# Kernel optimization log

Hardware: AMD Instinct MI355X
Metric: run time of the kernel (lower is better)

Reference implementation:

```python
import jax, jax.numpy as jnp
import numpy as np
from jax import lax

FILTER_SIZE = 11
N_ITER = 5


def gaussian_kernel1d(inv_theta, spacing, size):
    # distances = spacing * [-(size//2) .. size//2]; zero out center tap
    d = spacing * jnp.arange(-(size // 2), size // 2 + 1, dtype=jnp.float32)
    k = jnp.exp(-(d * inv_theta) ** 2 / 2)
    return k.at[size // 2].set(0.0)


def conv_along_axis(x, kernel, axis):
    # x: (C, *spatial); 1D conv along `axis`, 'same' padding (kernel symmetric -> corr == conv)
    x = jnp.moveaxis(x, axis, -1)
    shp = x.shape
    x2 = x.reshape(-1, 1, shp[-1])  # (M, 1, L)
    K = kernel.shape[0]
    out = lax.conv_general_dilated(
        x2, kernel[None, None, :].astype(x2.dtype), (1,), [(K // 2, K // 2)],
        dimension_numbers=('NCH', 'OIH', 'NCH'))
    return jnp.moveaxis(out.reshape(shp), -1, axis)


def _gaussian_filter_single(xi, inv_theta, spacing):
    # xi: (C, H, W); separable gaussian with per-sample spacing
    for i in range(2):
        k = gaussian_kernel1d(inv_theta[i], spacing[i], FILTER_SIZE)
        xi = conv_along_axis(xi, k, i + 1)
    return xi


_smooth = jax.vmap(_gaussian_filter_single, in_axes=(0, None, 0))


def reference(x, spatial_spacings, smoothness_weight, inv_smoothness_theta):
    n_classes = x.shape[1]
    comp = -jnp.eye(n_classes, dtype=x.dtype)  # -(label_i == label_j)
    negative_unary = x
    for _ in range(N_ITER):
        p = jax.nn.softmax(x, axis=1)
        s = smoothness_weight * _smooth(p, inv_smoothness_theta, spatial_spacings)
        c = jnp.einsum('bchw,cd->bdhw', s, comp)
        x = negative_unary - c
    return jax.nn.log_softmax(x, axis=1)


def setup_inputs() -> dict:
    key = jax.random.key(0)
    k1, = jax.random.split(key, 1)
    B, C, H, W = 16, 16, 384, 384
    return {
        'x': jax.random.normal(k1, (B, C, H, W), dtype=jnp.float32),
        'spatial_spacings': jnp.ones((B, 2), dtype=jnp.float32),
        'smoothness_weight': jnp.asarray(1.0, dtype=jnp.float32),
        'inv_smoothness_theta': jnp.ones((2,), dtype=jnp.float32),
    }
```

## Files before the change

### kernel.cpp

```cpp
#include <hip/hip_runtime.h>
#include <hip/hip_bf16.h>

#define BB 16
#define CC 16
#define HH 384
#define WW 384
#define HWSZ (HH*WW)
#define CHW (CC*HWSZ)
#define NPIX (BB*CHW)

#define FT 768
#define ROWS 12
#define HSEGS (HH/ROWS)
#define SROW 408

typedef unsigned short ushortT;

__device__ __forceinline__ void unpk2(unsigned u, float& lo, float& hi) {
    union { unsigned u; float f; } a, b;
    a.u = u << 16; b.u = u & 0xFFFF0000u;
    lo = a.f; hi = b.f;
}
__device__ __forceinline__ unsigned pk2(float lo, float hi) {
    __hip_bfloat162 h = __float22bfloat162_rn(make_float2(lo, hi));
    union { __hip_bfloat162 h; unsigned u; } c; c.h = h;
    return c.u;
}
__device__ __forceinline__ void unpk8(const uint4& q, float* v) {
    unpk2(q.x, v[0], v[1]); unpk2(q.y, v[2], v[3]);
    unpk2(q.z, v[4], v[5]); unpk2(q.w, v[6], v[7]);
}
__device__ __forceinline__ uint4 pk8(const float* v) {
    uint4 q;
    q.x = pk2(v[0], v[1]); q.y = pk2(v[2], v[3]);
    q.z = pk2(v[4], v[5]); q.w = pk2(v[6], v[7]);
    return q;
}
template<int CTRL>
__device__ __forceinline__ float dpp_f(float x) {
    union { float f; int i; } c; c.f = x;
    union { int i; float f; } r;
    r.i = __builtin_amdgcn_update_dpp(0, c.i, CTRL, 0xF, 0xF, true);
    return r.f;
}

template<int MODE>
__global__ __launch_bounds__(FT) void k_fused(
    const void* __restrict__ in0, const ushortT* __restrict__ x0b,
    void* __restrict__ outp, ushortT* __restrict__ x0b_out,
    const float* __restrict__ spacings, const float* __restrict__ invtheta,
    const float* __restrict__ swp)
{
    __shared__ ushortT xp[4][CC][SROW];
    __shared__ __align__(16) float l_lds[2][WW];

    const int t  = threadIdx.x;
    const int b  = blockIdx.y;
    const int h0 = blockIdx.x * ROWS;

    {
        const int buf = t / (CC * 12);
        const int rem = t - buf * (CC * 12);
        const int c = rem / 12, s = rem - (rem / 12) * 12;
        const int e = (s < 4) ? (2 * s) : (392 + 2 * (s - 4));
        *(unsigned*)&xp[buf][c][e] = 0u;
    }

    const float sw  = swp[0];
    const float sch = spacings[b * 2 + 0] * invtheta[0];
    const float scw = spacings[b * 2 + 1] * invtheta[1];
    float kh[5], kw[5];
#pragma unroll
    for (int j = 0; j < 5; ++j) {
        float dh = sch * (float)(j - 5); kh[j] = __expf(-0.5f * dh * dh);
        float dw = scw * (float)(j - 5); kw[j] = __expf(-0.5f * dw * dw);
    }

    const int ca = t / 48, ga = t - (t / 48) * 48;
    const int cp = t >> 2, qq = t & 3;

    const size_t cbase = (size_t)b * CHW + (size_t)ca * HWSZ + (size_t)ga * 8;
    const uint4 z4 = make_uint4(0u, 0u, 0u, 0u);

    uint4 W[12];
    if (MODE >= 1) {
        const ushortT* tin = (const ushortT*)in0;
#pragma unroll
        for (int j = 0; j < 12; ++j) {
            const int r = h0 + j - 5;
            W[j] = ((unsigned)r < HH) ? *(const uint4*)(tin + cbase + (size_t)r * WW) : z4;
        }
    }

    __syncthreads();

    auto A_row_m0 = [&](int h, int buf) {
        const float* xf = (const float*)in0;
        const float4 A0 = *(const float4*)(xf + cbase + (size_t)h * WW);
        const float4 A1 = *(const float4*)(xf + cbase + (size_t)h * WW + 4);
        float v[8] = {A0.x, A0.y, A0.z, A0.w, A1.x, A1.y, A1.z, A1.w};
        const uint4 q = pk8(v);
        *(uint4*)(x0b_out + cbase + (size_t)h * WW) = q;
        *(uint4*)&xp[buf][ca][8 + ga * 8] = q;
    };

    auto A_row = [&](int o, int buf, uint4 uq) {
        float acc[8];
#pragma unroll
        for (int k = 0; k < 8; ++k) acc[k] = 0.f;
#pragma unroll
        for (int j = 0; j < 5; ++j) {
            float e1[8], e2[8];
            unpk8(W[o + j], e1); unpk8(W[o + 10 - j], e2);
            const float kj = kh[j];
#pragma unroll
            for (int k = 0; k < 8; ++k) acc[k] = fmaf(kj, e1[k] + e2[k], acc[k]);
        }
        float uu[8]; unpk8(uq, uu);
        float xv[8];
#pragma unroll
        for (int k = 0; k < 8; ++k) xv[k] = fmaf(sw, acc[k], uu[k]);
        *(uint4*)&xp[buf][ca][8 + ga * 8] = pk8(xv);
    };

    auto B_row = [&](int buf, int r) {
        float xa[4], xb[4];
#pragma unroll
        for (int i = 0; i < 4; ++i) {
            const unsigned u = *(const unsigned*)&xp[buf][qq * 4 + i][8 + 2 * cp];
            unpk2(u, xa[i], xb[i]);
        }
        float m0 = fmaxf(fmaxf(xa[0], xa[1]), fmaxf(xa[2], xa[3]));
        float m1 = fmaxf(fmaxf(xb[0], xb[1]), fmaxf(xb[2], xb[3]));
        m0 = fmaxf(m0, dpp_f<0xB1>(m0)); m0 = fmaxf(m0, dpp_f<0x4E>(m0));
        m1 = fmaxf(m1, dpp_f<0xB1>(m1)); m1 = fmaxf(m1, dpp_f<0x4E>(m1));
        float e0[4], e1[4], s0 = 0.f, s1 = 0.f;
#pragma unroll
        for (int i = 0; i < 4; ++i) {
            e0[i] = __expf(xa[i] - m0); s0 += e0[i];
            e1[i] = __expf(xb[i] - m1); s1 += e1[i];
        }
        s0 += dpp_f<0xB1>(s0); s0 += dpp_f<0x4E>(s0);
        s1 += dpp_f<0xB1>(s1); s1 += dpp_f<0x4E>(s1);
        if (MODE <= 1) {
            const float i0 = 1.0f / s0, i1 = 1.0f / s1;
#pragma unroll
            for (int i = 0; i < 4; ++i)
                *(unsigned*)&xp[buf][qq * 4 + i][8 + 2 * cp] = pk2(e0[i] * i0, e1[i] * i1);
        } else {
            if (qq == 0) {
                l_lds[r][2 * cp]     = m0 + __logf(s0);
                l_lds[r][2 * cp + 1] = m1 + __logf(s1);
            }
        }
    };

    auto C_row = [&](int h, int buf, int r) {
        if (MODE <= 1) {
            const uint4 q0 = *(const uint4*)&xp[buf][ca][ga * 8];
            const uint4 q1 = *(const uint4*)&xp[buf][ca][ga * 8 + 8];
            const uint4 q2 = *(const uint4*)&xp[buf][ca][ga * 8 + 16];
            float w[24];
            unpk8(q0, w); unpk8(q1, w + 8); unpk8(q2, w + 16);
            float o[8];
#pragma unroll
            for (int k = 0; k < 8; ++k) {
                float a = 0.f;
#pragma unroll
                for (int j = 0; j < 5; ++j)
                    a = fmaf(kw[j], w[k + 3 + j] + w[k + 13 - j], a);
                o[k] = a;
            }
            *(uint4*)((ushortT*)outp + cbase + (size_t)h * WW) = pk8(o);
        } else {
            const uint4 xq = *(const uint4*)&xp[buf][ca][8 + ga * 8];
            float xv[8]; unpk8(xq, xv);
            const float4 l0 = *(const float4*)&l_lds[r][ga * 8];
            const float4 l1 = *(const float4*)&l_lds[r][ga * 8 + 4];
            float* op = (float*)outp + cbase + (size_t)h * WW;
            *(float4*)op       = make_float4(xv[0]-l0.x, xv[1]-l0.y, xv[2]-l0.z, xv[3]-l0.w);
            *(float4*)(op + 4) = make_float4(xv[4]-l1.x, xv[5]-l1.y, xv[6]-l1.z, xv[7]-l1.w);
        }
    };

#pragma unroll
    for (int p = 0; p < 6; ++p) {
        const int h  = h0 + 2 * p;
        const int bA = 2 * (p & 1);
        const int bC = 2 * ((p & 1) ^ 1);

        if (MODE == 0) {
            if (p > 0) { C_row(h - 2, bC, 0); C_row(h - 1, bC + 1, 1); }
            A_row_m0(h, bA); A_row_m0(h + 1, bA + 1);
        } else {
            if (p > 0) { C_row(h - 2, bC, 0); C_row(h - 1, bC + 1, 1); }
            const ushortT* tin = (const ushortT*)in0;
            const uint4 uq0 = *(const uint4*)(x0b + cbase + (size_t)h * WW);
            const uint4 uq1 = *(const uint4*)(x0b + cbase + (size_t)(h + 1) * WW);
            uint4 nt0 = z4, nt1 = z4;
            if (p < 5) {
                const int r0 = h + 7, r1 = h + 8;
                if (r0 < HH) nt0 = *(const uint4*)(tin + cbase + (size_t)r0 * WW);
                if (r1 < HH) nt1 = *(const uint4*)(tin + cbase + (size_t)r1 * WW);
            }
            A_row(0, bA,     uq0);
            A_row(1, bA + 1, uq1);
            if (p < 5) {
#pragma unroll
                for (int j = 0; j < 10; ++j) W[j] = W[j + 2];
                W[10] = nt0; W[11] = nt1;
            }
        }
        __syncthreads();

        B_row(bA, 0);
        B_row(bA + 1, 1);
        __syncthreads();
    }
    C_row(h0 + 10, 2, 0);
    C_row(h0 + 11, 3, 1);
}

extern "C" void kernel_launch(void* const* d_in, const int* in_sizes, int n_in,
                              void* d_out, int out_size, void* d_ws, size_t ws_size,
                              hipStream_t stream)
{
    const float* x0   = (const float*)d_in[0];
    const float* spac = (const float*)d_in[1];
    const float* sw   = (const float*)d_in[2];
    const float* it   = (const float*)d_in[3];

    ushortT* tA  = (ushortT*)d_ws;
    ushortT* tB  = tA + (size_t)NPIX;
    ushortT* x0b = tB + (size_t)NPIX;
    float*   out = (float*)d_out;

    dim3 gf(HSEGS, BB);
    dim3 bf(FT);

    k_fused<0><<<gf, bf, 0, stream>>>(x0, nullptr, tA, x0b, spac, it, sw);
    k_fused<1><<<gf, bf, 0, stream>>>(tA, x0b, tB, nullptr, spac, it, sw);
    k_fused<1><<<gf, bf, 0, stream>>>(tB, x0b, tA, nullptr, spac, it, sw);
    k_fused<1><<<gf, bf, 0, stream>>>(tA, x0b, tB, nullptr, spac, it, sw);
    k_fused<1><<<gf, bf, 0, stream>>>(tB, x0b, tA, nullptr, spac, it, sw);
    k_fused<2><<<gf, bf, 0, stream>>>(tA, x0b, out, nullptr, spac, it, sw);
}
```

Before: 408.1 us.

## Process four rows per pipeline stage with a ring-buffered register window

The per-block row pipeline now handles four rows per stage instead of two, so each 12-row segment runs in three groups and needs fewer block-wide barriers. LDS staging grows to eight row buffers and four logsumexp rows. The vertical-filter register window becomes a 16-entry ring indexed at compile time, which removes the per-step register shifting, and the prefetch of upcoming rows is issued earlier. The larger LDS footprint and wider register use may reduce occupancy; a launch-bounds hint of three blocks per SM is added to steer register allocation.

```diff
diff --git a/kernel.cpp b/kernel.cpp
--- a/kernel.cpp
+++ b/kernel.cpp
@@ -1,5 +1,6 @@
 #include <hip/hip_runtime.h>
 #include <hip/hip_bf16.h>
+#include <utility>
 
 #define BB 16
 #define CC 16
@@ -13,8 +14,10 @@
 #define ROWS 12
 #define HSEGS (HH/ROWS)
 #define SROW 408
+#define NBUF 8
 
 typedef unsigned short ushortT;
+template<int N> using ic = std::integral_constant<int, N>;
 
 __device__ __forceinline__ void unpk2(unsigned u, float& lo, float& hi) {
     union { unsigned u; float f; } a, b;
@@ -45,25 +48,29 @@
 }
 
 template<int MODE>
-__global__ __launch_bounds__(FT) void k_fused(
+__global__ __launch_bounds__(FT, 3) void k_fused(
     const void* __restrict__ in0, const ushortT* __restrict__ x0b,
     void* __restrict__ outp, ushortT* __restrict__ x0b_out,
     const float* __restrict__ spacings, const float* __restrict__ invtheta,
     const float* __restrict__ swp)
 {
-    __shared__ ushortT xp[4][CC][SROW];
-    __shared__ __align__(16) float l_lds[2][WW];
+    __shared__ ushortT xp[NBUF][CC][SROW];
+    __shared__ __align__(16) float l_lds[4][WW];
 
     const int t  = threadIdx.x;
     const int b  = blockIdx.y;
     const int h0 = blockIdx.x * ROWS;
 
     {
-        const int buf = t / (CC * 12);
-        const int rem = t - buf * (CC * 12);
-        const int c = rem / 12, s = rem - (rem / 12) * 12;
-        const int e = (s < 4) ? (2 * s) : (392 + 2 * (s - 4));
-        *(unsigned*)&xp[buf][c][e] = 0u;
+#pragma unroll
+        for (int z = 0; z < 2; ++z) {
+            const int idx = t + z * FT;
+            const int buf = idx / (CC * 12);
+            const int rem = idx - buf * (CC * 12);
+            const int c = rem / 12, s = rem - (rem / 12) * 12;
+            const int e = (s < 4) ? (2 * s) : (392 + 2 * (s - 4));
+            *(unsigned*)&xp[buf][c][e] = 0u;
+        }
     }
 
     const float sw  = swp[0];
@@ -82,46 +89,18 @@
     const size_t cbase = (size_t)b * CHW + (size_t)ca * HWSZ + (size_t)ga * 8;
     const uint4 z4 = make_uint4(0u, 0u, 0u, 0u);
 
-    uint4 W[12];
+    uint4 W[16];
     if (MODE >= 1) {
         const ushortT* tin = (const ushortT*)in0;
 #pragma unroll
-        for (int j = 0; j < 12; ++j) {
-            const int r = h0 + j - 5;
-            W[j] = ((unsigned)r < HH) ? *(const uint4*)(tin + cbase + (size_t)r * WW) : z4;
-        }
+        for (int s = 0; s < 14; ++s) {
+            const int r = h0 + s - 5;
+            W[s] = ((unsigned)r < HH) ? *(const uint4*)(tin + cbase + (size_t)r * WW) : z4;
+        }
+        W[14] = z4; W[15] = z4;
     }
 
     __syncthreads();
-
-    auto A_row_m0 = [&](int h, int buf) {
-        const float* xf = (const float*)in0;
-        const float4 A0 = *(const float4*)(xf + cbase + (size_t)h * WW);
-        const float4 A1 = *(const float4*)(xf + cbase + (size_t)h * WW + 4);
-        float v[8] = {A0.x, A0.y, A0.z, A0.w, A1.x, A1.y, A1.z, A1.w};
-        const uint4 q = pk8(v);
-        *(uint4*)(x0b_out + cbase + (size_t)h * WW) = q;
-        *(uint4*)&xp[buf][ca][8 + ga * 8] = q;
-    };
-
-    auto A_row = [&](int o, int buf, uint4 uq) {
-        float acc[8];
-#pragma unroll
-        for (int k = 0; k < 8; ++k) acc[k] = 0.f;
-#pragma unroll
-        for (int j = 0; j < 5; ++j) {
-            float e1[8], e2[8];
-            unpk8(W[o + j], e1); unpk8(W[o + 10 - j], e2);
-            const float kj = kh[j];
-#pragma unroll
-            for (int k = 0; k < 8; ++k) acc[k] = fmaf(kj, e1[k] + e2[k], acc[k]);
-        }
-        float uu[8]; unpk8(uq, uu);
-        float xv[8];
-#pragma unroll
-        for (int k = 0; k < 8; ++k) xv[k] = fmaf(sw, acc[k], uu[k]);
-        *(uint4*)&xp[buf][ca][8 + ga * 8] = pk8(xv);
-    };
 
     auto B_row = [&](int buf, int r) {
         float xa[4], xb[4];
@@ -183,42 +162,89 @@
         }
     };
 
-#pragma unroll
-    for (int p = 0; p < 6; ++p) {
-        const int h  = h0 + 2 * p;
-        const int bA = 2 * (p & 1);
-        const int bC = 2 * ((p & 1) ^ 1);
+    auto A_row = [&](auto Ic, int buf, const uint4& uq) {
+        constexpr int i = decltype(Ic)::value;
+        float acc[8];
+#pragma unroll
+        for (int k = 0; k < 8; ++k) acc[k] = 0.f;
+#pragma unroll
+        for (int j = 0; j < 5; ++j) {
+            const int sa = (i + j) % 16;
+            const int sb = (i + 10 - j) % 16;
+            float e1[8], e2[8];
+            unpk8(W[sa], e1); unpk8(W[sb], e2);
+            const float kj = kh[j];
+#pragma unroll
+            for (int k = 0; k < 8; ++k)
+                acc[k] = fmaf(kj, e1[k] + e2[k], acc[k]);
+        }
+        float uu[8]; unpk8(uq, uu);
+        float xv[8];
+#pragma unroll
+        for (int k = 0; k < 8; ++k) xv[k] = fmaf(sw, acc[k], uu[k]);
+        *(uint4*)&xp[buf][ca][8 + ga * 8] = pk8(xv);
+    };
+
+    auto A_row_m0 = [&](int h, int buf) {
+        const float* xf = (const float*)in0;
+        const float4 A0 = *(const float4*)(xf + cbase + (size_t)h * WW);
+        const float4 A1 = *(const float4*)(xf + cbase + (size_t)h * WW + 4);
+        float v[8] = {A0.x, A0.y, A0.z, A0.w, A1.x, A1.y, A1.z, A1.w};
+        const uint4 q = pk8(v);
+        *(uint4*)(x0b_out + cbase + (size_t)h * WW) = q;
+        *(uint4*)&xp[buf][ca][8 + ga * 8] = q;
+    };
+
+    auto group = [&](auto Gc) {
+        constexpr int g = decltype(Gc)::value;
+        const int h = h0 + 4 * g;
+        constexpr int bufA = (g & 1) * 4;
+        constexpr int bufC = ((g & 1) ^ 1) * 4;
 
         if (MODE == 0) {
-            if (p > 0) { C_row(h - 2, bC, 0); C_row(h - 1, bC + 1, 1); }
-            A_row_m0(h, bA); A_row_m0(h + 1, bA + 1);
+            if (g > 0) {
+#pragma unroll
+                for (int k = 0; k < 4; ++k) C_row(h - 4 + k, bufC + k, k);
+            }
+#pragma unroll
+            for (int k = 0; k < 4; ++k) A_row_m0(h + k, bufA + k);
         } else {
-            if (p > 0) { C_row(h - 2, bC, 0); C_row(h - 1, bC + 1, 1); }
             const ushortT* tin = (const ushortT*)in0;
-            const uint4 uq0 = *(const uint4*)(x0b + cbase + (size_t)h * WW);
-            const uint4 uq1 = *(const uint4*)(x0b + cbase + (size_t)(h + 1) * WW);
-            uint4 nt0 = z4, nt1 = z4;
-            if (p < 5) {
-                const int r0 = h + 7, r1 = h + 8;
-                if (r0 < HH) nt0 = *(const uint4*)(tin + cbase + (size_t)r0 * WW);
-                if (r1 < HH) nt1 = *(const uint4*)(tin + cbase + (size_t)r1 * WW);
-            }
-            A_row(0, bA,     uq0);
-            A_row(1, bA + 1, uq1);
-            if (p < 5) {
-#pragma unroll
-                for (int j = 0; j < 10; ++j) W[j] = W[j + 2];
-                W[10] = nt0; W[11] = nt1;
+            uint4 uq[4];
+#pragma unroll
+            for (int k = 0; k < 4; ++k)
+                uq[k] = *(const uint4*)(x0b + cbase + (size_t)(h + k) * WW);
+            uint4 nt[4] = {z4, z4, z4, z4};
+            if (g < 2) {
+#pragma unroll
+                for (int k = 0; k < 4; ++k) {
+                    const int r = h + 9 + k;
+                    if (r < HH) nt[k] = *(const uint4*)(tin + cbase + (size_t)r * WW);
+                }
+            }
+            if (g > 0) {
+#pragma unroll
+                for (int k = 0; k < 4; ++k) C_row(h - 4 + k, bufC + k, k);
+            }
+            A_row(ic<4 * g + 0>{}, bufA + 0, uq[0]);
+            A_row(ic<4 * g + 1>{}, bufA + 1, uq[1]);
+            A_row(ic<4 * g + 2>{}, bufA + 2, uq[2]);
+            A_row(ic<4 * g + 3>{}, bufA + 3, uq[3]);
+            if (g < 2) {
+#pragma unroll
+                for (int k = 0; k < 4; ++k) W[(4 * g + 14 + k) % 16] = nt[k];
             }
         }
         __syncthreads();
-
-        B_row(bA, 0);
-        B_row(bA + 1, 1);
+        B_row(bufA + 0, 0); B_row(bufA + 1, 1);
+        B_row(bufA + 2, 2); B_row(bufA + 3, 3);
         __syncthreads();
-    }
-    C_row(h0 + 10, 2, 0);
-    C_row(h0 + 11, 3, 1);
+    };
+
+    group(ic<0>{}); group(ic<1>{}); group(ic<2>{});
+
+#pragma unroll
+    for (int k = 0; k < 4; ++k) C_row(h0 + 8 + k, k, k);
 }
 
 extern "C" void kernel_launch(void* const* d_in, const int* in_sizes, int n_in,
```

Measured after the change: 685.5 us. +68.0%, slower.
